# Kernel optimization log

Measured on AMD Instinct MI355X. Metric: run time of the kernel, lower is better.

## Reference

```python
import jax, jax.numpy as jnp
import numpy as np

N_FFT = 1024
HOP = 256
BATCH = 16
SAMPLES = 262144


def hann_window(n):
    # torch.hann_window default (periodic=True): 0.5 * (1 - cos(2*pi*k/n))
    k = jnp.arange(n, dtype=jnp.float32)
    return 0.5 - 0.5 * jnp.cos(2.0 * jnp.pi * k / n)


def setup_inputs() -> dict:
    key = jax.random.key(0)
    x = jax.random.normal(key, (BATCH, SAMPLES), dtype=jnp.float32)
    window = hann_window(N_FFT)  # (n_fft,)
    return {"x": x, "window": window}


def reference(x, window):
    # Faithful STFT.forward: pad -> frame (identity-kernel conv1d == gather) ->
    # window -> rfft along the frame axis; norm=None.
    pad = N_FFT - HOP
    pad_left = pad // 2
    xp = jnp.pad(x, ((0, 0), (pad_left, pad - pad_left)))
    n_frames = (xp.shape[1] - N_FFT) // HOP + 1
    # gather-based framing, equivalent to conv1d with eye(n_fft) kernel, stride=hop
    idx = jnp.arange(n_frames)[:, None] * HOP + jnp.arange(N_FFT)[None, :]  # (frames, n_fft)
    frames = xp[:, idx]                       # (B, frames, n_fft)
    frames = frames * window[None, None, :]   # windowing
    spec = jnp.fft.rfft(frames, axis=-1)      # (B, frames, n_bins)
    real = jnp.transpose(spec.real, (0, 2, 1))  # (B, n_bins, frames)
    imag = jnp.transpose(spec.imag, (0, 2, 1))
    return real, imag
```

## Files before the change

### kernel.cpp

```cpp
#include <hip/hip_runtime.h>

#define HOP      256
#define SAMPLES  262144
#define NBINS    513
#define NFRAMES  1024
#define FPB      16

__device__ __forceinline__ float2 cmul(float2 a, float2 b) {
  return make_float2(a.x * b.x - a.y * b.y, a.x * b.y + a.y * b.x);
}

__device__ __forceinline__ float2 lds_ld(const float2* p, int bo) {
  return *(const float2*)((const char*)p + bo);
}
__device__ __forceinline__ void lds_st(float2* p, int bo, float2 v) {
  *(float2*)((char*)p + bo) = v;
}

__device__ __forceinline__ int swz(int c) {
  int H = c >> 6, M = (c >> 3) & 7, L = c & 7;
  return (H << 6) | ((M ^ (H & 1)) << 3) | (L ^ M);
}

__device__ __forceinline__ void fft8(float2 v[8]) {
  const float R = 0.70710678118654752440f;
  float2 s0 = make_float2(v[0].x + v[4].x, v[0].y + v[4].y);
  float2 d0 = make_float2(v[0].x - v[4].x, v[0].y - v[4].y);
  float2 s1 = make_float2(v[1].x + v[5].x, v[1].y + v[5].y);
  float2 d1 = make_float2(v[1].x - v[5].x, v[1].y - v[5].y);
  float2 s2 = make_float2(v[2].x + v[6].x, v[2].y + v[6].y);
  float2 d2 = make_float2(v[2].x - v[6].x, v[2].y - v[6].y);
  float2 s3 = make_float2(v[3].x + v[7].x, v[3].y + v[7].y);
  float2 d3 = make_float2(v[3].x - v[7].x, v[3].y - v[7].y);
  float2 e1 = make_float2(R * (d1.x + d1.y), R * (d1.y - d1.x));
  float2 e2 = make_float2(d2.y, -d2.x);
  float2 e3 = make_float2(R * (d3.y - d3.x), R * (-d3.x - d3.y));
  float2 p0 = make_float2(s0.x + s2.x, s0.y + s2.y);
  float2 q0 = make_float2(s0.x - s2.x, s0.y - s2.y);
  float2 p1 = make_float2(s1.x + s3.x, s1.y + s3.y);
  float2 q1 = make_float2(s1.x - s3.x, s1.y - s3.y);
  float2 q1t = make_float2(q1.y, -q1.x);
  float2 p2 = make_float2(d0.x + e2.x, d0.y + e2.y);
  float2 q2 = make_float2(d0.x - e2.x, d0.y - e2.y);
  float2 p3 = make_float2(e1.x + e3.x, e1.y + e3.y);
  float2 q3 = make_float2(e1.x - e3.x, e1.y - e3.y);
  float2 q3t = make_float2(q3.y, -q3.x);
  v[0] = make_float2(p0.x + p1.x, p0.y + p1.y);
  v[4] = make_float2(p0.x - p1.x, p0.y - p1.y);
  v[2] = make_float2(q0.x + q1t.x, q0.y + q1t.y);
  v[6] = make_float2(q0.x - q1t.x, q0.y - q1t.y);
  v[1] = make_float2(p2.x + p3.x, p2.y + p3.y);
  v[5] = make_float2(p2.x - p3.x, p2.y - p3.y);
  v[3] = make_float2(q2.x + q3t.x, q2.y + q3t.y);
  v[7] = make_float2(q2.x - q3t.x, q2.y - q3t.y);
}

__global__ __launch_bounds__(1024, 8)
void stft_kernel(const float* __restrict__ x, const float* __restrict__ win,
                 float* __restrict__ out) {
  __shared__ float2 z[FPB * 512];
  const int t  = threadIdx.x;
  const int b  = blockIdx.x >> 6;
  const int f0 = (blockIdx.x & 63) * FPB;

  {
    const int w = t >> 6;
    const int u = t & 63;
    const int g = u >> 3, m2l = u & 7;
    float2* zf = z + (w << 9);

    const int A0    = (g << 3) | (m2l ^ g);
    const int B1w_e = (A0 ^ w) << 3;
    const int B1w_o = B1w_e ^ 64;
    const int C1    = (g << 6) | ((g & 1) << 3) | m2l;
    const int B1r   = (C1 ^ w) << 3;
    const int D0    = (g << 6) | ((m2l ^ (g & 1)) << 3) | m2l;
    const int B2r   = (D0 ^ w) << 3;
    const int F0    = (m2l << 3) | (g ^ m2l);
    const int B3_e  = (F0 ^ w) << 3;
    const int B3_o  = B3_e ^ 64;

    const float* xb = x + (size_t)b * SAMPLES;
    const int fr   = f0 + w;
    const int base = fr * HOP - 384;
    float2 r[8];
    if (f0 != 0 && f0 != (NFRAMES - FPB)) {
      const float2* xc = (const float2*)(xb + base);
      const float2* wc = (const float2*)win;
#pragma unroll
      for (int n1 = 0; n1 < 8; ++n1) {
        float2 xv = xc[(n1 << 6) + u];
        float2 wv = wc[(n1 << 6) + u];
        r[n1] = make_float2(xv.x * wv.x, xv.y * wv.y);
      }
    } else {
#pragma unroll
      for (int n1 = 0; n1 < 8; ++n1) {
        int s = (n1 << 7) + 2 * u;
        int idx = base + s;
        float2 xv = make_float2(0.f, 0.f);
        if (idx >= 0 && idx < SAMPLES) xv = *(const float2*)(xb + idx);
        float2 wv = *(const float2*)(win + s);
        r[n1] = make_float2(xv.x * wv.x, xv.y * wv.y);
      }
    }

    fft8(r);
    float sn, cs;
    __sincosf((float)u * (-6.28318530717958647693f / 512.f), &sn, &cs);
    {
      float2 w1 = make_float2(cs, sn);
      float2 w2 = cmul(w1, w1);
      float2 w3 = cmul(w2, w1);
      float2 w4 = cmul(w2, w2);
      r[1] = cmul(r[1], w1);
      r[2] = cmul(r[2], w2);
      r[3] = cmul(r[3], w3);
      r[4] = cmul(r[4], w4);
      r[5] = cmul(r[5], cmul(w4, w1));
      r[6] = cmul(r[6], cmul(w4, w2));
      r[7] = cmul(r[7], cmul(w4, w3));
    }
    lds_st(zf, B1w_e,        r[0]);
    lds_st(zf, B1w_o +  512, r[1]);
    lds_st(zf, B1w_e + 1024, r[2]);
    lds_st(zf, B1w_o + 1536, r[3]);
    lds_st(zf, B1w_e + 2048, r[4]);
    lds_st(zf, B1w_o + 2560, r[5]);
    lds_st(zf, B1w_e + 3072, r[6]);
    lds_st(zf, B1w_o + 3584, r[7]);

    float2 y[8];
#pragma unroll
    for (int m1 = 0; m1 < 8; ++m1) y[m1] = lds_ld(zf, B1r ^ (72 * m1));

    fft8(y);
    __sincosf((float)m2l * (-6.28318530717958647693f / 64.f), &sn, &cs);
    {
      float2 w1 = make_float2(cs, sn);
      float2 w2 = cmul(w1, w1);
      float2 w3 = cmul(w2, w1);
      float2 w4 = cmul(w2, w2);
      y[1] = cmul(y[1], w1);
      y[2] = cmul(y[2], w2);
      y[3] = cmul(y[3], w3);
      y[4] = cmul(y[4], w4);
      y[5] = cmul(y[5], cmul(w4, w1));
      y[6] = cmul(y[6], cmul(w4, w2));
      y[7] = cmul(y[7], cmul(w4, w3));
    }
#pragma unroll
    for (int j1 = 0; j1 < 8; ++j1) lds_st(zf, B1r ^ (72 * j1), y[j1]);

    float2 h[8];
#pragma unroll
    for (int m = 0; m < 8; ++m) h[m] = lds_ld(zf, B2r ^ (m << 3));

    fft8(h);
    lds_st(zf, B3_e,        h[0]);
    lds_st(zf, B3_o +  512, h[1]);
    lds_st(zf, B3_e + 1024, h[2]);
    lds_st(zf, B3_o + 1536, h[3]);
    lds_st(zf, B3_e + 2048, h[4]);
    lds_st(zf, B3_o + 2560, h[5]);
    lds_st(zf, B3_e + 3072, h[6]);
    lds_st(zf, B3_o + 3584, h[7]);
  }
  __syncthreads();

  {
    const int f  = t & 15;
    const int q  = t >> 4;
    const int fr = f0 + f;
    const float2* zq = z + (f << 9);
    const int G    = ((q >> 3) << 3) | ((q & 7) ^ (q >> 3));
    const int BK_e = (G ^ f) << 3;
    const int BK_o = BK_e ^ 64;
    float* out_r = out;
    float* out_i = out + (size_t)16 * NBINS * NFRAMES;
    float sn, cs;
    __sincosf((float)q * (-6.28318530717958647693f / 1024.f), &sn, &cs);
    float2 tw = make_float2(cs, sn);
    const float2 stp = make_float2(0.92387953251128675613f, -0.38268343236508977173f);
#pragma unroll
    for (int i = 0; i < 5; ++i) {
      int k = q + (i << 6);
      if (k > 256) break;
      float2 Zk = lds_ld(zq, ((i & 1) ? BK_o : BK_e) + i * 512);
      int mk = (512 - k) & 511;
      float2 Zm = lds_ld(zq, (swz(mk) ^ f) << 3);
      float xer  = 0.5f * (Zk.x + Zm.x);
      float xei  = 0.5f * (Zk.y - Zm.y);
      float xor_ = 0.5f * (Zk.y + Zm.y);
      float xoi  = -0.5f * (Zk.x - Zm.x);
      float ur = tw.x * xor_ - tw.y * xoi;
      float ui = tw.x * xoi + tw.y * xor_;
      size_t o1 = ((size_t)b * NBINS + k) * NFRAMES + fr;
      size_t o2 = ((size_t)b * NBINS + (512 - k)) * NFRAMES + fr;
      out_r[o1] = xer + ur;
      out_i[o1] = xei + ui;
      out_r[o2] = xer - ur;
      out_i[o2] = ui - xei;
      tw = cmul(tw, stp);
    }
  }
}

extern "C" void kernel_launch(void* const* d_in, const int* in_sizes, int n_in,
                              void* d_out, int out_size, void* d_ws, size_t ws_size,
                              hipStream_t stream) {
  const float* x = (const float*)d_in[0];
  const float* w = (const float*)d_in[1];
  float* out = (float*)d_out;
  (void)in_sizes; (void)n_in; (void)out_size; (void)d_ws; (void)ws_size;
  stft_kernel<<<dim3(1024), dim3(1024), 0, stream>>>(x, w, out);
}
```

Baseline: 24.56 us.

## Make blocks persistent over four frame tiles with double-buffered LDS pipelining

```diff
diff --git a/kernel.cpp b/kernel.cpp
--- a/kernel.cpp
+++ b/kernel.cpp
@@ -4,19 +4,16 @@
 #define SAMPLES  262144
 #define NBINS    513
 #define NFRAMES  1024
-#define FPB      16
 
 __device__ __forceinline__ float2 cmul(float2 a, float2 b) {
   return make_float2(a.x * b.x - a.y * b.y, a.x * b.y + a.y * b.x);
 }
-
 __device__ __forceinline__ float2 lds_ld(const float2* p, int bo) {
   return *(const float2*)((const char*)p + bo);
 }
 __device__ __forceinline__ void lds_st(float2* p, int bo, float2 v) {
   *(float2*)((char*)p + bo) = v;
 }
-
 __device__ __forceinline__ int swz(int c) {
   int H = c >> 6, M = (c >> 3) & 7, L = c & 7;
   return (H << 6) | ((M ^ (H & 1)) << 3) | (L ^ M);
@@ -55,153 +52,199 @@
   v[7] = make_float2(q2.x - q3t.x, q2.y - q3t.y);
 }
 
-__global__ __launch_bounds__(1024, 8)
+#define UNP(J, ZB, IK, IM, TW, XR1, XI1, XR2, XI2) {                 \
+    const int ff = fb + (J);                                         \
+    float2 Zk = lds_ld(ZB, (((ff) << 9) + ((IK) ^ (ff))) << 3);      \
+    float2 Zm = lds_ld(ZB, (((ff) << 9) + ((IM) ^ (ff))) << 3);      \
+    float xer  = 0.5f * (Zk.x + Zm.x);                               \
+    float xei  = 0.5f * (Zk.y - Zm.y);                               \
+    float xo_r = 0.5f * (Zk.y + Zm.y);                               \
+    float xo_i = -0.5f * (Zk.x - Zm.x);                              \
+    float ur = (TW).x * xo_r - (TW).y * xo_i;                        \
+    float ui = (TW).x * xo_i + (TW).y * xo_r;                        \
+    XR1 = xer + ur; XI1 = xei + ui; XR2 = xer - ur; XI2 = ui - xei; }
+
+__global__ __launch_bounds__(1024, 4)
 void stft_kernel(const float* __restrict__ x, const float* __restrict__ win,
                  float* __restrict__ out) {
-  __shared__ float2 z[FPB * 512];
-  const int t  = threadIdx.x;
-  const int b  = blockIdx.x >> 6;
-  const int f0 = (blockIdx.x & 63) * FPB;
-
-  {
-    const int w = t >> 6;
-    const int u = t & 63;
-    const int g = u >> 3, m2l = u & 7;
-    float2* zf = z + (w << 9);
-
-    const int A0    = (g << 3) | (m2l ^ g);
-    const int B1w_e = (A0 ^ w) << 3;
-    const int B1w_o = B1w_e ^ 64;
-    const int C1    = (g << 6) | ((g & 1) << 3) | m2l;
-    const int B1r   = (C1 ^ w) << 3;
-    const int D0    = (g << 6) | ((m2l ^ (g & 1)) << 3) | m2l;
-    const int B2r   = (D0 ^ w) << 3;
-    const int F0    = (m2l << 3) | (g ^ m2l);
-    const int B3_e  = (F0 ^ w) << 3;
-    const int B3_o  = B3_e ^ 64;
-
-    const float* xb = x + (size_t)b * SAMPLES;
-    const int fr   = f0 + w;
+  __shared__ float2 z[2 * 8192];
+
+  const int t    = threadIdx.x;
+  const int bid  = blockIdx.x;
+  const int b    = bid >> 4;
+  const int tile0 = (bid & 15) << 2;
+  const float* xb = x + (size_t)b * SAMPLES;
+  float* out_r = out;
+  float* out_i = out + (size_t)16 * NBINS * NFRAMES;
+
+  const int w   = t >> 6;
+  const int u   = t & 63;
+  const int g   = u >> 3, m2l = u & 7;
+  const int A0    = (g << 3) | (m2l ^ g);
+  const int B1w_e = (A0 ^ w) << 3;
+  const int B1w_o = B1w_e ^ 64;
+  const int C1    = (g << 6) | ((g & 1) << 3) | m2l;
+  const int B1r   = (C1 ^ w) << 3;
+  const int D0    = (g << 6) | ((m2l ^ (g & 1)) << 3) | m2l;
+  const int B2r   = (D0 ^ w) << 3;
+  const int F0    = (m2l << 3) | (g ^ m2l);
+  const int B3_e  = (F0 ^ w) << 3;
+  const int B3_o  = B3_e ^ 64;
+
+  float sn, cs;
+  __sincosf((float)u * (-6.28318530717958647693f / 512.f), &sn, &cs);
+  float2 s1w1 = make_float2(cs, sn);
+  float2 s1w2 = cmul(s1w1, s1w1);
+  float2 s1w3 = cmul(s1w2, s1w1);
+  float2 s1w4 = cmul(s1w2, s1w2);
+  float2 s1w5 = cmul(s1w4, s1w1);
+  float2 s1w6 = cmul(s1w4, s1w2);
+  float2 s1w7 = cmul(s1w4, s1w3);
+  __sincosf((float)m2l * (-6.28318530717958647693f / 64.f), &sn, &cs);
+  float2 s2w1 = make_float2(cs, sn);
+  float2 s2w2 = cmul(s2w1, s2w1);
+  float2 s2w3 = cmul(s2w2, s2w1);
+  float2 s2w4 = cmul(s2w2, s2w2);
+  float2 s2w5 = cmul(s2w4, s2w1);
+  float2 s2w6 = cmul(s2w4, s2w2);
+  float2 s2w7 = cmul(s2w4, s2w3);
+
+  const int g4 = t & 3;
+  const int fb = g4 << 2;
+  const int q  = t >> 2;
+  const int ik = swz(q);
+  const int im = swz((512 - q) & 511);
+  __sincosf((float)q * (-6.28318530717958647693f / 1024.f), &sn, &cs);
+  const float2 twq = make_float2(cs, sn);
+  const size_t rowA = ((size_t)b * NBINS + q) * NFRAMES + fb;
+  const size_t rowB = ((size_t)b * NBINS + (512 - q)) * NFRAMES + fb;
+
+  for (int s = 0; s < 4; ++s) {
+    const int f0s  = (tile0 + s) << 4;
+    const int fr   = f0s + w;
     const int base = fr * HOP - 384;
-    float2 r[8];
-    if (f0 != 0 && f0 != (NFRAMES - FPB)) {
+    float2 rr[8];
+    if (fr >= 2 && fr <= 1021) {
       const float2* xc = (const float2*)(xb + base);
       const float2* wc = (const float2*)win;
 #pragma unroll
       for (int n1 = 0; n1 < 8; ++n1) {
         float2 xv = xc[(n1 << 6) + u];
         float2 wv = wc[(n1 << 6) + u];
-        r[n1] = make_float2(xv.x * wv.x, xv.y * wv.y);
+        rr[n1] = make_float2(xv.x * wv.x, xv.y * wv.y);
       }
     } else {
 #pragma unroll
       for (int n1 = 0; n1 < 8; ++n1) {
-        int s = (n1 << 7) + 2 * u;
-        int idx = base + s;
+        int sidx = (n1 << 7) + 2 * u;
+        int idx = base + sidx;
         float2 xv = make_float2(0.f, 0.f);
         if (idx >= 0 && idx < SAMPLES) xv = *(const float2*)(xb + idx);
-        float2 wv = *(const float2*)(win + s);
-        r[n1] = make_float2(xv.x * wv.x, xv.y * wv.y);
+        float2 wv = *(const float2*)(win + sidx);
+        rr[n1] = make_float2(xv.x * wv.x, xv.y * wv.y);
       }
     }
 
-    fft8(r);
-    float sn, cs;
-    __sincosf((float)u * (-6.28318530717958647693f / 512.f), &sn, &cs);
+    if (s > 0) {
+      const float2* zb = z + (((s - 1) & 1) << 13);
+      const int f0p = (tile0 + s - 1) << 4;
+      float r1x, r1y, r1z, r1w, i1x, i1y, i1z, i1w;
+      float r2x, r2y, r2z, r2w, i2x, i2y, i2z, i2w;
+      UNP(0, zb, ik, im, twq, r1x, i1x, r2x, i2x)
+      UNP(1, zb, ik, im, twq, r1y, i1y, r2y, i2y)
+      UNP(2, zb, ik, im, twq, r1z, i1z, r2z, i2z)
+      UNP(3, zb, ik, im, twq, r1w, i1w, r2w, i2w)
+      *(float4*)(out_r + rowA + f0p) = make_float4(r1x, r1y, r1z, r1w);
+      *(float4*)(out_i + rowA + f0p) = make_float4(i1x, i1y, i1z, i1w);
+      *(float4*)(out_r + rowB + f0p) = make_float4(r2x, r2y, r2z, r2w);
+      *(float4*)(out_i + rowB + f0p) = make_float4(i2x, i2y, i2z, i2w);
+      if (q == 0) {
+        const int ik6 = swz(256);
+        const float2 tw6 = make_float2(0.f, -1.f);
+        float a0, a1, a2, a3, c0, c1, c2, c3, d_, e_;
+        UNP(0, zb, ik6, ik6, tw6, a0, c0, d_, e_)
+        UNP(1, zb, ik6, ik6, tw6, a1, c1, d_, e_)
+        UNP(2, zb, ik6, ik6, tw6, a2, c2, d_, e_)
+        UNP(3, zb, ik6, ik6, tw6, a3, c3, d_, e_)
+        size_t o6 = ((size_t)b * NBINS + 256) * NFRAMES + fb + f0p;
+        *(float4*)(out_r + o6) = make_float4(a0, a1, a2, a3);
+        *(float4*)(out_i + o6) = make_float4(c0, c1, c2, c3);
+      }
+    }
+
     {
-      float2 w1 = make_float2(cs, sn);
-      float2 w2 = cmul(w1, w1);
-      float2 w3 = cmul(w2, w1);
-      float2 w4 = cmul(w2, w2);
-      r[1] = cmul(r[1], w1);
-      r[2] = cmul(r[2], w2);
-      r[3] = cmul(r[3], w3);
-      r[4] = cmul(r[4], w4);
-      r[5] = cmul(r[5], cmul(w4, w1));
-      r[6] = cmul(r[6], cmul(w4, w2));
-      r[7] = cmul(r[7], cmul(w4, w3));
-    }
-    lds_st(zf, B1w_e,        r[0]);
-    lds_st(zf, B1w_o +  512, r[1]);
-    lds_st(zf, B1w_e + 1024, r[2]);
-    lds_st(zf, B1w_o + 1536, r[3]);
-    lds_st(zf, B1w_e + 2048, r[4]);
-    lds_st(zf, B1w_o + 2560, r[5]);
-    lds_st(zf, B1w_e + 3072, r[6]);
-    lds_st(zf, B1w_o + 3584, r[7]);
-
-    float2 y[8];
-#pragma unroll
-    for (int m1 = 0; m1 < 8; ++m1) y[m1] = lds_ld(zf, B1r ^ (72 * m1));
-
-    fft8(y);
-    __sincosf((float)m2l * (-6.28318530717958647693f / 64.f), &sn, &cs);
-    {
-      float2 w1 = make_float2(cs, sn);
-      float2 w2 = cmul(w1, w1);
-      float2 w3 = cmul(w2, w1);
-      float2 w4 = cmul(w2, w2);
-      y[1] = cmul(y[1], w1);
-      y[2] = cmul(y[2], w2);
-      y[3] = cmul(y[3], w3);
-      y[4] = cmul(y[4], w4);
-      y[5] = cmul(y[5], cmul(w4, w1));
-      y[6] = cmul(y[6], cmul(w4, w2));
-      y[7] = cmul(y[7], cmul(w4, w3));
-    }
-#pragma unroll
-    for (int j1 = 0; j1 < 8; ++j1) lds_st(zf, B1r ^ (72 * j1), y[j1]);
-
-    float2 h[8];
-#pragma unroll
-    for (int m = 0; m < 8; ++m) h[m] = lds_ld(zf, B2r ^ (m << 3));
-
-    fft8(h);
-    lds_st(zf, B3_e,        h[0]);
-    lds_st(zf, B3_o +  512, h[1]);
-    lds_st(zf, B3_e + 1024, h[2]);
-    lds_st(zf, B3_o + 1536, h[3]);
-    lds_st(zf, B3_e + 2048, h[4]);
-    lds_st(zf, B3_o + 2560, h[5]);
-    lds_st(zf, B3_e + 3072, h[6]);
-    lds_st(zf, B3_o + 3584, h[7]);
+      float2* zf = z + ((s & 1) << 13) + (w << 9);
+      fft8(rr);
+      rr[1] = cmul(rr[1], s1w1);
+      rr[2] = cmul(rr[2], s1w2);
+      rr[3] = cmul(rr[3], s1w3);
+      rr[4] = cmul(rr[4], s1w4);
+      rr[5] = cmul(rr[5], s1w5);
+      rr[6] = cmul(rr[6], s1w6);
+      rr[7] = cmul(rr[7], s1w7);
+      lds_st(zf, B1w_e,        rr[0]);
+      lds_st(zf, B1w_o +  512, rr[1]);
+      lds_st(zf, B1w_e + 1024, rr[2]);
+      lds_st(zf, B1w_o + 1536, rr[3]);
+      lds_st(zf, B1w_e + 2048, rr[4]);
+      lds_st(zf, B1w_o + 2560, rr[5]);
+      lds_st(zf, B1w_e + 3072, rr[6]);
+      lds_st(zf, B1w_o + 3584, rr[7]);
+
+      float2 y[8];
+#pragma unroll
+      for (int m1 = 0; m1 < 8; ++m1) y[m1] = lds_ld(zf, B1r ^ (72 * m1));
+      fft8(y);
+      y[1] = cmul(y[1], s2w1);
+      y[2] = cmul(y[2], s2w2);
+      y[3] = cmul(y[3], s2w3);
+      y[4] = cmul(y[4], s2w4);
+      y[5] = cmul(y[5], s2w5);
+      y[6] = cmul(y[6], s2w6);
+      y[7] = cmul(y[7], s2w7);
+#pragma unroll
+      for (int j1 = 0; j1 < 8; ++j1) lds_st(zf, B1r ^ (72 * j1), y[j1]);
+
+      float2 h[8];
+#pragma unroll
+      for (int m = 0; m < 8; ++m) h[m] = lds_ld(zf, B2r ^ (m << 3));
+      fft8(h);
+      lds_st(zf, B3_e,        h[0]);
+      lds_st(zf, B3_o +  512, h[1]);
+      lds_st(zf, B3_e + 1024, h[2]);
+      lds_st(zf, B3_o + 1536, h[3]);
+      lds_st(zf, B3_e + 2048, h[4]);
+      lds_st(zf, B3_o + 2560, h[5]);
+      lds_st(zf, B3_e + 3072, h[6]);
+      lds_st(zf, B3_o + 3584, h[7]);
+    }
+    __syncthreads();
   }
-  __syncthreads();
 
   {
-    const int f  = t & 15;
-    const int q  = t >> 4;
-    const int fr = f0 + f;
-    const float2* zq = z + (f << 9);
-    const int G    = ((q >> 3) << 3) | ((q & 7) ^ (q >> 3));
-    const int BK_e = (G ^ f) << 3;
-    const int BK_o = BK_e ^ 64;
-    float* out_r = out;
-    float* out_i = out + (size_t)16 * NBINS * NFRAMES;
-    float sn, cs;
-    __sincosf((float)q * (-6.28318530717958647693f / 1024.f), &sn, &cs);
-    float2 tw = make_float2(cs, sn);
-    const float2 stp = make_float2(0.92387953251128675613f, -0.38268343236508977173f);
-#pragma unroll
-    for (int i = 0; i < 5; ++i) {
-      int k = q + (i << 6);
-      if (k > 256) break;
-      float2 Zk = lds_ld(zq, ((i & 1) ? BK_o : BK_e) + i * 512);
-      int mk = (512 - k) & 511;
-      float2 Zm = lds_ld(zq, (swz(mk) ^ f) << 3);
-      float xer  = 0.5f * (Zk.x + Zm.x);
-      float xei  = 0.5f * (Zk.y - Zm.y);
-      float xor_ = 0.5f * (Zk.y + Zm.y);
-      float xoi  = -0.5f * (Zk.x - Zm.x);
-      float ur = tw.x * xor_ - tw.y * xoi;
-      float ui = tw.x * xoi + tw.y * xor_;
-      size_t o1 = ((size_t)b * NBINS + k) * NFRAMES + fr;
-      size_t o2 = ((size_t)b * NBINS + (512 - k)) * NFRAMES + fr;
-      out_r[o1] = xer + ur;
-      out_i[o1] = xei + ui;
-      out_r[o2] = xer - ur;
-      out_i[o2] = ui - xei;
-      tw = cmul(tw, stp);
+    const float2* zb = z + ((3 & 1) << 13);
+    const int f0p = (tile0 + 3) << 4;
+    float r1x, r1y, r1z, r1w, i1x, i1y, i1z, i1w;
+    float r2x, r2y, r2z, r2w, i2x, i2y, i2z, i2w;
+    UNP(0, zb, ik, im, twq, r1x, i1x, r2x, i2x)
+    UNP(1, zb, ik, im, twq, r1y, i1y, r2y, i2y)
+    UNP(2, zb, ik, im, twq, r1z, i1z, r2z, i2z)
+    UNP(3, zb, ik, im, twq, r1w, i1w, r2w, i2w)
+    *(float4*)(out_r + rowA + f0p) = make_float4(r1x, r1y, r1z, r1w);
+    *(float4*)(out_i + rowA + f0p) = make_float4(i1x, i1y, i1z, i1w);
+    *(float4*)(out_r + rowB + f0p) = make_float4(r2x, r2y, r2z, r2w);
+    *(float4*)(out_i + rowB + f0p) = make_float4(i2x, i2y, i2z, i2w);
+    if (q == 0) {
+      const int ik6 = swz(256);
+      const float2 tw6 = make_float2(0.f, -1.f);
+      float a0, a1, a2, a3, c0, c1, c2, c3, d_, e_;
+      UNP(0, zb, ik6, ik6, tw6, a0, c0, d_, e_)
+      UNP(1, zb, ik6, ik6, tw6, a1, c1, d_, e_)
+      UNP(2, zb, ik6, ik6, tw6, a2, c2, d_, e_)
+      UNP(3, zb, ik6, ik6, tw6, a3, c3, d_, e_)
+      size_t o6 = ((size_t)b * NBINS + 256) * NFRAMES + fb + f0p;
+      *(float4*)(out_r + o6) = make_float4(a0, a1, a2, a3);
+      *(float4*)(out_i + o6) = make_float4(c0, c1, c2, c3);
     }
   }
 }
@@ -213,5 +256,5 @@
   const float* w = (const float*)d_in[1];
   float* out = (float*)d_out;
   (void)in_sizes; (void)n_in; (void)out_size; (void)d_ws; (void)ws_size;
-  stft_kernel<<<dim3(1024), dim3(1024), 0, stream>>>(x, w, out);
-}
+  stft_kernel<<<dim3(256), dim3(1024), 0, stream>>>(x, w, out);
+}
```

After: 51.77 us. 111% more time.
